# Optimization experiments

Hardware: AMD Instinct MI355X
Metric: run time of the kernel (lower is better)

## Reference

```python
import jax, jax.numpy as jnp
import numpy as np

NH, NKV, HD, H = 32, 8, 128, 4096
G = NH // NKV  # GQA group size = 4
EPS = 1e-5
SCALE = HD ** -0.5


def rms_norm(x, w, eps=EPS):
    # per-head RMSNorm over last dim, computed in fp32
    xf = x.astype(jnp.float32)
    var = jnp.mean(xf * xf, axis=-1, keepdims=True)
    return (w * (xf * jax.lax.rsqrt(var + eps)).astype(x.dtype))


def setup_inputs() -> dict:
    key = jax.random.key(0)
    ks = jax.random.split(key, 4)
    B, SQ, SKV = 4, 1024, 1601
    return {
        "hidden_states": jax.random.normal(ks[0], (B, SQ, H), jnp.float32),
        "cross_attention_states": jax.random.normal(ks[1], (B, SKV, H), jnp.float32),
        "wqkv": jax.random.normal(ks[2], ((NH + 2 * NKV) * HD, H), jnp.float32) * 0.02,
        "wo": jax.random.normal(ks[3], (NH * HD, H), jnp.float32) * 0.02,
        "q_norm_weight": jnp.ones((HD,), jnp.float32),
        "k_norm_weight": jnp.ones((HD,), jnp.float32),
    }


def reference(hidden_states, cross_attention_states, wqkv, wo, q_norm_weight, k_norm_weight):
    B, SQ, _ = hidden_states.shape
    SKV = cross_attention_states.shape[1]
    q_sz, kv_sz = NH * HD, NKV * HD

    # fused QKV projection on decoder tokens -> keep only q
    qkv_dec = jnp.einsum('bsh,oh->bso', hidden_states, wqkv)
    q = qkv_dec[..., :q_sz]
    # fused QKV projection on encoder tokens -> keep only k, v
    qkv_enc = jnp.einsum('bsh,oh->bso', cross_attention_states, wqkv)
    k = qkv_enc[..., q_sz:q_sz + kv_sz]
    v = qkv_enc[..., q_sz + kv_sz:]

    q = rms_norm(q.reshape(B, SQ, NH, HD), q_norm_weight)      # [B,SQ,NH,HD]
    k = rms_norm(k.reshape(B, SKV, NKV, HD), k_norm_weight)    # [B,SKV,NKV,HD]
    v = v.reshape(B, SKV, NKV, HD)

    # GQA: group query heads per kv head
    qg = q.reshape(B, SQ, NKV, G, HD)
    scores = jnp.einsum('bqkgd,bskd->bkgqs', qg, k) * SCALE    # [B,NKV,G,SQ,SKV]
    probs = jax.nn.softmax(scores, axis=-1)
    out = jnp.einsum('bkgqs,bskd->bqkgd', probs, v)            # [B,SQ,NKV,G,HD]
    out = out.reshape(B, SQ, NH * HD)
    return jnp.einsum('bso,ho->bsh', out, wo.T.T) if False else jnp.einsum('bsf,hf->bsh', out, wo)
```

## Files before the change

kernel.cpp:

```cpp
#include <hip/hip_runtime.h>
#include <cstdint>
#include <math.h>

typedef _Float16 f16;
typedef __attribute__((ext_vector_type(4))) _Float16 f16x4;
typedef __attribute__((ext_vector_type(8))) _Float16 f16x8;
typedef __attribute__((ext_vector_type(4))) float f32x4;

__device__ inline void gload_lds16(const void* g, void* l) {
  auto gp = reinterpret_cast<const __attribute__((address_space(1))) uint32_t*>(
      reinterpret_cast<uintptr_t>(g));
  auto lp = reinterpret_cast<__attribute__((address_space(3))) uint32_t*>(
      reinterpret_cast<uintptr_t>(l));
  __builtin_amdgcn_global_load_lds(gp, lp, 16 , 0, 0);
}

__device__ inline float wave_sum64(float v) {
#pragma unroll
  for (int m = 1; m < 64; m <<= 1) v += __shfl_xor(v, m);
  return v;
}

__global__ __launch_bounds__(256) void cvt_kernel(const float* __restrict__ src,
                                                  f16* __restrict__ dst, int n4) {
  int idx = blockIdx.x * blockDim.x + threadIdx.x;
  int stride = gridDim.x * blockDim.x;
  for (int i = idx; i < n4; i += stride) {
    float4 v = reinterpret_cast<const float4*>(src)[i];
    f16x4 h;
    h.x = (f16)v.x; h.y = (f16)v.y; h.z = (f16)v.z; h.w = (f16)v.w;
    reinterpret_cast<f16x4*>(dst)[i] = h;
  }
}

template <bool MB, int EPI>
__global__ __launch_bounds__(512, 2) void gemm256(const f16* __restrict__ A,
                                                  const f16* __restrict__ Bw,
                                                  float* __restrict__ C,
                                                  f16* __restrict__ Ch,
                                                  const float* __restrict__ wvec,
                                                  int M, int N, int K) {
  __shared__ f16 As[2][256][64];
  __shared__ f16 Bs[2][256][64];
  const int tid = threadIdx.x;
  const int l = tid & 63, w = tid >> 6;
  const int lq = l & 15, lk = l >> 4;
  const int wm = w >> 2, wn = w & 3;
  const int nwg = gridDim.x * gridDim.y;
  const int p = blockIdx.y * gridDim.x + blockIdx.x;
  const int L = (p & 7) * (nwg >> 3) + (p >> 3);
  const int bx = L % gridDim.x, by = L / gridDim.x;
  const int brow = by * 256, bcol = bx * 256;
  const int KT = K >> 6;

  const int srow8 = w * 8 + (l >> 3);
  const int scol  = ((l & 7) ^ (l >> 3)) * 8;
  const int swz   = (lq & 7) << 4;

  f32x4 acc[8][4];
  f32x4 zf = {0.f, 0.f, 0.f, 0.f};
#pragma unroll
  for (int m = 0; m < 8; ++m)
#pragma unroll
    for (int n = 0; n < 4; ++n) acc[m][n] = zf;

  auto stageA = [&](int kt, int buf, int i) {
    int ra = brow + i * 64 + srow8;
    if (MB) ra = (ra < M) ? ra : (M - 1);
    gload_lds16(A + (size_t)ra * K + kt * 64 + scol,
                (char*)(&As[buf][0][0]) + i * 8192 + w * 1024);
  };
  auto stageB = [&](int kt, int buf, int i) {
    int rb = bcol + i * 64 + srow8;
    gload_lds16(Bw + (size_t)rb * K + kt * 64 + scol,
                (char*)(&Bs[buf][0][0]) + i * 8192 + w * 1024);
  };
  auto ldA = [&](int buf, int m, int kk) -> f16x8 {
    int r = wm * 128 + m * 16 + lq;
    return *reinterpret_cast<const f16x8*>(
        (char*)(&As[buf][0][0]) + r * 128 + ((kk * 64 + lk * 16) ^ swz));
  };
  auto ldB = [&](int buf, int n, int kk) -> f16x8 {
    int r = wn * 64 + n * 16 + lq;
    return *reinterpret_cast<const f16x8*>(
        (char*)(&Bs[buf][0][0]) + r * 128 + ((kk * 64 + lk * 16) ^ swz));
  };

#pragma unroll
  for (int i = 0; i < 4; ++i) stageA(0, 0, i);
#pragma unroll
  for (int i = 0; i < 4; ++i) stageB(0, 0, i);

  f16x8 av[4][2], bv[2][2];
  for (int t = 0; t < KT; ++t) {
    const int buf = t & 1, nbuf = buf ^ 1;
    const bool pf = (t + 1 < KT);

    if (pf) { stageA(t + 1, nbuf, 0); stageA(t + 1, nbuf, 1); }
    if (pf) asm volatile("s_waitcnt vmcnt(2)" ::: "memory");
    else    asm volatile("s_waitcnt vmcnt(0)" ::: "memory");
    __builtin_amdgcn_s_barrier();
#pragma unroll
    for (int mm = 0; mm < 4; ++mm)
#pragma unroll
      for (int kk = 0; kk < 2; ++kk) av[mm][kk] = ldA(buf, mm, kk);
#pragma unroll
    for (int nn = 0; nn < 2; ++nn)
#pragma unroll
      for (int kk = 0; kk < 2; ++kk) bv[nn][kk] = ldB(buf, nn, kk);
    __builtin_amdgcn_s_setprio(1);
#pragma unroll
    for (int mm = 0; mm < 4; ++mm)
#pragma unroll
      for (int nn = 0; nn < 2; ++nn)
#pragma unroll
        for (int kk = 0; kk < 2; ++kk)
          acc[mm][nn] = __builtin_amdgcn_mfma_f32_16x16x32_f16(av[mm][kk], bv[nn][kk], acc[mm][nn], 0, 0, 0);
    __builtin_amdgcn_s_setprio(0);
    asm volatile("" ::: "memory");
    __builtin_amdgcn_s_barrier();

#pragma unroll
    for (int mm = 0; mm < 4; ++mm)
#pragma unroll
      for (int kk = 0; kk < 2; ++kk) av[mm][kk] = ldA(buf, 4 + mm, kk);
    if (pf) { stageA(t + 1, nbuf, 2); stageA(t + 1, nbuf, 3); }
    asm volatile("" ::: "memory");
    __builtin_amdgcn_s_barrier();
    __builtin_amdgcn_s_setprio(1);
#pragma unroll
    for (int mm = 0; mm < 4; ++mm)
#pragma unroll
      for (int nn = 0; nn < 2; ++nn)
#pragma unroll
        for (int kk = 0; kk < 2; ++kk)
          acc[4 + mm][nn] = __builtin_amdgcn_mfma_f32_16x16x32_f16(av[mm][kk], bv[nn][kk], acc[4 + mm][nn], 0, 0, 0);
    __builtin_amdgcn_s_setprio(0);
    asm volatile("" ::: "memory");
    __builtin_amdgcn_s_barrier();

#pragma unroll
    for (int nn = 0; nn < 2; ++nn)
#pragma unroll
      for (int kk = 0; kk < 2; ++kk) bv[nn][kk] = ldB(buf, 2 + nn, kk);
    if (pf) { stageB(t + 1, nbuf, 0); stageB(t + 1, nbuf, 1); }
    asm volatile("" ::: "memory");
    __builtin_amdgcn_s_barrier();
    __builtin_amdgcn_s_setprio(1);
#pragma unroll
    for (int mm = 0; mm < 4; ++mm)
#pragma unroll
      for (int nn = 0; nn < 2; ++nn)
#pragma unroll
        for (int kk = 0; kk < 2; ++kk)
          acc[4 + mm][2 + nn] = __builtin_amdgcn_mfma_f32_16x16x32_f16(av[mm][kk], bv[nn][kk], acc[4 + mm][2 + nn], 0, 0, 0);
    __builtin_amdgcn_s_setprio(0);
    asm volatile("" ::: "memory");
    __builtin_amdgcn_s_barrier();

#pragma unroll
    for (int mm = 0; mm < 4; ++mm)
#pragma unroll
      for (int kk = 0; kk < 2; ++kk) av[mm][kk] = ldA(buf, mm, kk);
    if (pf) { stageB(t + 1, nbuf, 2); stageB(t + 1, nbuf, 3); }
    asm volatile("" ::: "memory");
    __builtin_amdgcn_s_barrier();
    __builtin_amdgcn_s_setprio(1);
#pragma unroll
    for (int mm = 0; mm < 4; ++mm)
#pragma unroll
      for (int nn = 0; nn < 2; ++nn)
#pragma unroll
        for (int kk = 0; kk < 2; ++kk)
          acc[mm][2 + nn] = __builtin_amdgcn_mfma_f32_16x16x32_f16(av[mm][kk], bv[nn][kk], acc[mm][2 + nn], 0, 0, 0);
    __builtin_amdgcn_s_setprio(0);
    asm volatile("" ::: "memory");
    __builtin_amdgcn_s_barrier();
  }

  if (EPI == 0) {
#pragma unroll
    for (int m = 0; m < 8; ++m) {
#pragma unroll
      for (int j = 0; j < 4; ++j) {
        int row = brow + wm * 128 + m * 16 + lk * 4 + j;
        if (MB && row >= M) continue;
        float* dst = C + (size_t)row * N + bcol + wn * 64 + lq;
#pragma unroll
        for (int n = 0; n < 4; ++n) dst[n * 16] = acc[m][n][j];
      }
    }
  } else {
    __shared__ float ssq[256][4];
#pragma unroll
    for (int m = 0; m < 8; ++m)
#pragma unroll
      for (int j = 0; j < 4; ++j) {
        int lr = wm * 128 + m * 16 + lk * 4 + j;
        float pp = 0.f;
#pragma unroll
        for (int n = 0; n < 4; ++n) pp += acc[m][n][j] * acc[m][n][j];
        pp += __shfl_xor(pp, 1);
        pp += __shfl_xor(pp, 2);
        pp += __shfl_xor(pp, 4);
        pp += __shfl_xor(pp, 8);
        if (lq == 0) ssq[lr][wn] = pp;
      }
    asm volatile("" ::: "memory");
    __builtin_amdgcn_s_barrier();
    const int hh = wn >> 1;
    float wv[4];
#pragma unroll
    for (int n = 0; n < 4; ++n) wv[n] = wvec[(wn * 64 + n * 16 + lq) & 127];
#pragma unroll
    for (int m = 0; m < 8; ++m)
#pragma unroll
      for (int j = 0; j < 4; ++j) {
        int lr = wm * 128 + m * 16 + lk * 4 + j;
        float ss = ssq[lr][hh * 2] + ssq[lr][hh * 2 + 1];
        float rs = rsqrtf(ss * (1.0f / 128.0f) + 1e-5f) *
                   (0.08838834764831845f * 1.4426950408889634f);
        f16* dst = Ch + (size_t)(brow + lr) * N + bcol + wn * 64 + lq;
#pragma unroll
        for (int n = 0; n < 4; ++n) dst[n * 16] = (f16)(acc[m][n][j] * rs * wv[n]);
      }
  }
}

__global__ __launch_bounds__(256) void kvscatter_kernel(const float* __restrict__ KVraw,
                                                        const float* __restrict__ wk,
                                                        f16* __restrict__ Kf,
                                                        f16* __restrict__ Vtf) {
  const int w = threadIdx.x >> 6, l = threadIdx.x & 63;
  const int gw = blockIdx.x * 4 + w;
  const int r = gw >> 3, kvh = gw & 7;
  const int b = r / 1601, s = r - b * 1601;
  const float* kr = KVraw + (size_t)r * 2048 + kvh * 128;
  float2 kx = reinterpret_cast<const float2*>(kr)[l];
  float ss = wave_sum64(kx.x * kx.x + kx.y * kx.y);
  float rs = rsqrtf(ss * (1.0f / 128.0f) + 1e-5f);
  float2 wv = reinterpret_cast<const float2*>(wk)[l];
  union { f16 h[2]; unsigned u; } pk;
  pk.h[0] = (f16)(kx.x * rs * wv.x);
  pk.h[1] = (f16)(kx.y * rs * wv.y);
  reinterpret_cast<unsigned*>(Kf + ((size_t)(b * 8 + kvh) * 1664 + s) * 128)[l] = pk.u;
  const float* vr = kr + 1024;
  float2 vx = reinterpret_cast<const float2*>(vr)[l];
  f16* vcol = Vtf + ((size_t)(b * 8 + kvh) * 128 + l * 2) * 1664 + s;
  vcol[0] = (f16)vx.x;
  vcol[1664] = (f16)vx.y;
}

__global__ __launch_bounds__(512, 4) void attn_kernel(const f16* __restrict__ Qf,
                                                      const f16* __restrict__ Kf,
                                                      const f16* __restrict__ Vtf,
                                                      f16* __restrict__ Oa) {
  __shared__ f16 Ksm[2][64][128];
  __shared__ f16 Vsm[2][128][64];
  __shared__ f16 Psm[8][16][64];
  const int p = blockIdx.x;
  const int L = (p & 7) * 128 + (p >> 3);
  const int qt = L & 7, h = (L >> 3) & 31, b = L >> 8;
  const int kvh = h >> 2;
  const int tid = threadIdx.x;
  const int l = tid & 63, w = tid >> 6;
  const int lq = l & 15, lk = l >> 4;

  f16x8 qreg[4];
  const f16* Qbase = Qf + ((size_t)(b * 1024 + qt * 128 + w * 16)) * 4096 + h * 128;
#pragma unroll
  for (int ks = 0; ks < 4; ++ks)
    qreg[ks] = *reinterpret_cast<const f16x8*>(
        Qbase + (size_t)lq * 4096 + ks * 32 + lk * 8);

  const f16* Kb = Kf + (size_t)(b * 8 + kvh) * (1664 * 128);
  const f16* Vb = Vtf + (size_t)(b * 8 + kvh) * (128 * 1664);

  f32x4 o[8];
  f32x4 zf = {0.f, 0.f, 0.f, 0.f};
#pragma unroll
  for (int dn = 0; dn < 8; ++dn) o[dn] = zf;
  float mrow[4], lrow[4];
#pragma unroll
  for (int j = 0; j < 4; ++j) { mrow[j] = -1e30f; lrow[j] = 0.f; }

  char* Pw = (char*)(&Psm[w][0][0]);
  const int swzR = (lq & 7) << 4;

  auto stageK = [&](int t, int buf) {
#pragma unroll
    for (int i = 0; i < 2; ++i) {
      int row = w * 8 + i * 4 + lk;
      int cb = (lq * 16) ^ ((row & 7) << 4);
      gload_lds16(Kb + (size_t)(t * 64 + row) * 128 + (cb >> 1),
                  (char*)(&Ksm[buf][0][0]) + w * 2048 + i * 1024);
    }
  };
  auto stageV = [&](int t, int buf) {
#pragma unroll
    for (int i = 0; i < 2; ++i) {
      int r = w * 16 + i * 8 + (l >> 3);
      int cb = ((l & 7) * 16) ^ ((r & 7) << 4);
      gload_lds16(Vb + (size_t)r * 1664 + t * 64 + (cb >> 1),
                  (char*)(&Vsm[buf][0][0]) + w * 2048 + i * 1024);
    }
  };

  stageK(0, 0);
  stageV(0, 0);
  int cur = 0;
  for (int t = 0; t < 26; ++t) {
    if (t < 25) {
      stageK(t + 1, cur ^ 1);
      stageV(t + 1, cur ^ 1);
      asm volatile("s_waitcnt vmcnt(4)" ::: "memory");
    } else {
      asm volatile("s_waitcnt vmcnt(0)" ::: "memory");
    }
    __builtin_amdgcn_s_barrier();

    f32x4 s[4];
#pragma unroll
    for (int kn = 0; kn < 4; ++kn) s[kn] = zf;
    __builtin_amdgcn_s_setprio(1);
#pragma unroll
    for (int ks = 0; ks < 4; ++ks) {
      f16x8 bf[4];
#pragma unroll
      for (int kn = 0; kn < 4; ++kn)
        bf[kn] = *reinterpret_cast<const f16x8*>(
            (char*)(&Ksm[cur][0][0]) + (kn * 16 + lq) * 256 + ((ks * 64 + lk * 16) ^ swzR));
#pragma unroll
      for (int kn = 0; kn < 4; ++kn)
        s[kn] = __builtin_amdgcn_mfma_f32_16x16x32_f16(qreg[ks], bf[kn], s[kn], 0, 0, 0);
    }
    __builtin_amdgcn_s_setprio(0);

    if (t == 25) {
#pragma unroll
      for (int kn = 0; kn < 4; ++kn) {
        bool valid = (kn * 16 + lq) < 1;
#pragma unroll
        for (int j = 0; j < 4; ++j) s[kn][j] = valid ? s[kn][j] : -1e30f;
      }
    }

#pragma unroll
    for (int j = 0; j < 4; ++j) {
      float mt = fmaxf(fmaxf(s[0][j], s[1][j]), fmaxf(s[2][j], s[3][j]));
      mt = fmaxf(mt, __shfl_xor(mt, 1));
      mt = fmaxf(mt, __shfl_xor(mt, 2));
      mt = fmaxf(mt, __shfl_xor(mt, 4));
      mt = fmaxf(mt, __shfl_xor(mt, 8));
      float mo = mrow[j];
      if (mt > mo + 8.0f) {
        float corr = exp2f(mo - mt);
        mrow[j] = mt;
        lrow[j] *= corr;
#pragma unroll
        for (int dn = 0; dn < 8; ++dn) o[dn][j] *= corr;
        mo = mt;
      }
      float rsum = 0.f;
#pragma unroll
      for (int kn = 0; kn < 4; ++kn) {
        float pv = exp2f(s[kn][j] - mo);
        s[kn][j] = pv;
        rsum += pv;
      }
      lrow[j] += rsum;
      int prow = lk * 4 + j;
      int swzW = (prow & 7) << 4;
#pragma unroll
      for (int kn = 0; kn < 4; ++kn)
        *reinterpret_cast<f16*>(Pw + prow * 128 + (((kn * 16 + lq) * 2) ^ swzW)) =
            (f16)s[kn][j];
    }

    __builtin_amdgcn_s_setprio(1);
#pragma unroll
    for (int c = 0; c < 2; ++c) {
      f16x8 pa = *reinterpret_cast<const f16x8*>(
          Pw + lq * 128 + ((c * 64 + lk * 16) ^ swzR));
      f16x8 vb[8];
#pragma unroll
      for (int dn = 0; dn < 8; ++dn)
        vb[dn] = *reinterpret_cast<const f16x8*>(
            (char*)(&Vsm[cur][0][0]) + (dn * 16 + lq) * 128 + ((c * 64 + lk * 16) ^ swzR));
#pragma unroll
      for (int dn = 0; dn < 8; ++dn)
        o[dn] = __builtin_amdgcn_mfma_f32_16x16x32_f16(pa, vb[dn], o[dn], 0, 0, 0);
    }
    __builtin_amdgcn_s_setprio(0);
    __builtin_amdgcn_s_barrier();
    cur ^= 1;
  }

#pragma unroll
  for (int j = 0; j < 4; ++j) {
    float fl = lrow[j];
    fl += __shfl_xor(fl, 1);
    fl += __shfl_xor(fl, 2);
    fl += __shfl_xor(fl, 4);
    fl += __shfl_xor(fl, 8);
    float il = 1.0f / fl;
    int token = b * 1024 + qt * 128 + w * 16 + lk * 4 + j;
    f16* dst = Oa + (size_t)token * 4096 + h * 128;
#pragma unroll
    for (int dn = 0; dn < 8; ++dn) dst[dn * 16 + lq] = (f16)(o[dn][j] * il);
  }
}

extern "C" void kernel_launch(void* const* d_in, const int* in_sizes, int n_in,
                              void* d_out, int out_size, void* d_ws, size_t ws_size,
                              hipStream_t stream) {
  const float* hidden = (const float*)d_in[0];
  const float* cross  = (const float*)d_in[1];
  const float* wqkv   = (const float*)d_in[2];
  const float* wo     = (const float*)d_in[3];
  const float* qw     = (const float*)d_in[4];
  const float* kw     = (const float*)d_in[5];

  char* ws = (char*)d_ws;
  f16* hidden_h = (f16*)(ws + 0);
  f16* attn_h   = hidden_h;
  f16* wqkv_h = (f16*)(ws + 33554432);
  f16* cross_h = (f16*)(ws + 83886080);
  f16* k_h     = cross_h;
  f16* vt_h    = (f16*)(ws + 83886080 + 13631488);
  float* kvraw = (float*)(ws + 136347648);
  f16* wo_h    = (f16*)(ws + 136347648);
  f16* q_h = (f16*)d_out;

  cvt_kernel<<<2048, 256, 0, stream>>>(hidden, hidden_h, 16777216 / 4);
  cvt_kernel<<<2048, 256, 0, stream>>>(cross, cross_h, 26230784 / 4);
  cvt_kernel<<<2048, 256, 0, stream>>>(wqkv, wqkv_h, 25165824 / 4);
  gemm256<true, 0><<<dim3(8, 26), 512, 0, stream>>>(
      cross_h, wqkv_h + (size_t)4096 * 4096, kvraw, nullptr, nullptr, 6404, 2048, 4096);
  hipMemsetAsync(ws + 83886080, 0, 27262976, stream);
  kvscatter_kernel<<<12808, 256, 0, stream>>>(kvraw, kw, k_h, vt_h);
  cvt_kernel<<<2048, 256, 0, stream>>>(wo, wo_h, 16777216 / 4);
  gemm256<false, 1><<<dim3(16, 16), 512, 0, stream>>>(
      hidden_h, wqkv_h, nullptr, q_h, qw, 4096, 4096, 4096);
  attn_kernel<<<1024, 512, 0, stream>>>(q_h, k_h, vt_h, attn_h);
  gemm256<false, 0><<<dim3(16, 16), 512, 0, stream>>>(
      attn_h, wo_h, (float*)d_out, nullptr, nullptr, 4096, 4096, 4096);
}
```

Before: 685.1 us.

## Fuse K/V norm and scatter into GEMM epilogue and merge conversion launches

The KV projection GEMM epilogue now applies the K RMSNorm and writes K and transposed V directly in fp16 layout. This removes the fp32 intermediate buffer and the separate scatter kernel. The three fp32-to-fp16 conversions and the memset are merged into one kernel. The epilogue's V stores are strided, and register pressure in the GEMM may rise.

```diff
diff --git a/kernel.cpp b/kernel.cpp
--- a/kernel.cpp
+++ b/kernel.cpp
@@ -15,10 +15,23 @@
   __builtin_amdgcn_global_load_lds(gp, lp, 16 , 0, 0);
 }
 
-__device__ inline float wave_sum64(float v) {
-#pragma unroll
-  for (int m = 1; m < 64; m <<= 1) v += __shfl_xor(v, m);
-  return v;
+__global__ __launch_bounds__(256) void cvtzero_kernel(const float* __restrict__ s0, f16* __restrict__ d0,
+                                                      const float* __restrict__ s1, f16* __restrict__ d1,
+                                                      const float* __restrict__ s2, f16* __restrict__ d2,
+                                                      float4* __restrict__ z) {
+  int idx = blockIdx.x * blockDim.x + threadIdx.x;
+  int stride = gridDim.x * blockDim.x;
+  for (int i = idx; i < 18747392; i += stride) {
+    const float* src; f16* dst; int k;
+    if (i < 4194304) { src = s0; dst = d0; k = i; }
+    else if (i < 10752000) { src = s1; dst = d1; k = i - 4194304; }
+    else if (i < 17043456) { src = s2; dst = d2; k = i - 10752000; }
+    else { float4 zr = {0.f, 0.f, 0.f, 0.f}; z[i - 17043456] = zr; continue; }
+    float4 v = reinterpret_cast<const float4*>(src)[k];
+    f16x4 h;
+    h.x = (f16)v.x; h.y = (f16)v.y; h.z = (f16)v.z; h.w = (f16)v.w;
+    reinterpret_cast<f16x4*>(dst)[k] = h;
+  }
 }
 
 __global__ __launch_bounds__(256) void cvt_kernel(const float* __restrict__ src,
@@ -39,6 +52,7 @@
                                                   float* __restrict__ C,
                                                   f16* __restrict__ Ch,
                                                   const float* __restrict__ wvec,
+                                                  f16* __restrict__ Vtf,
                                                   int M, int N, int K) {
   __shared__ f16 As[2][256][64];
   __shared__ f16 Bs[2][256][64];
@@ -190,7 +204,7 @@
         for (int n = 0; n < 4; ++n) dst[n * 16] = acc[m][n][j];
       }
     }
-  } else {
+  } else if (EPI == 1) {
     __shared__ float ssq[256][4];
 #pragma unroll
     for (int m = 0; m < 8; ++m)
@@ -224,31 +238,65 @@
 #pragma unroll
         for (int n = 0; n < 4; ++n) dst[n * 16] = (f16)(acc[m][n][j] * rs * wv[n]);
       }
-  }
-}
-
-__global__ __launch_bounds__(256) void kvscatter_kernel(const float* __restrict__ KVraw,
-                                                        const float* __restrict__ wk,
-                                                        f16* __restrict__ Kf,
-                                                        f16* __restrict__ Vtf) {
-  const int w = threadIdx.x >> 6, l = threadIdx.x & 63;
-  const int gw = blockIdx.x * 4 + w;
-  const int r = gw >> 3, kvh = gw & 7;
-  const int b = r / 1601, s = r - b * 1601;
-  const float* kr = KVraw + (size_t)r * 2048 + kvh * 128;
-  float2 kx = reinterpret_cast<const float2*>(kr)[l];
-  float ss = wave_sum64(kx.x * kx.x + kx.y * kx.y);
-  float rs = rsqrtf(ss * (1.0f / 128.0f) + 1e-5f);
-  float2 wv = reinterpret_cast<const float2*>(wk)[l];
-  union { f16 h[2]; unsigned u; } pk;
-  pk.h[0] = (f16)(kx.x * rs * wv.x);
-  pk.h[1] = (f16)(kx.y * rs * wv.y);
-  reinterpret_cast<unsigned*>(Kf + ((size_t)(b * 8 + kvh) * 1664 + s) * 128)[l] = pk.u;
-  const float* vr = kr + 1024;
-  float2 vx = reinterpret_cast<const float2*>(vr)[l];
-  f16* vcol = Vtf + ((size_t)(b * 8 + kvh) * 128 + l * 2) * 1664 + s;
-  vcol[0] = (f16)vx.x;
-  vcol[1664] = (f16)vx.y;
+  } else {
+    const bool isK = (bcol < 1024);
+    __shared__ float ssq[256][4];
+    if (isK) {
+#pragma unroll
+      for (int m = 0; m < 8; ++m)
+#pragma unroll
+        for (int j = 0; j < 4; ++j) {
+          int lr = wm * 128 + m * 16 + lk * 4 + j;
+          float pp = 0.f;
+#pragma unroll
+          for (int n = 0; n < 4; ++n) pp += acc[m][n][j] * acc[m][n][j];
+          pp += __shfl_xor(pp, 1);
+          pp += __shfl_xor(pp, 2);
+          pp += __shfl_xor(pp, 4);
+          pp += __shfl_xor(pp, 8);
+          if (lq == 0) ssq[lr][wn] = pp;
+        }
+      asm volatile("" ::: "memory");
+      __builtin_amdgcn_s_barrier();
+    }
+    const int hh = wn >> 1;
+    float wv[4];
+    if (isK) {
+#pragma unroll
+      for (int n = 0; n < 4; ++n) wv[n] = wvec[(wn * 64 + n * 16 + lq) & 127];
+    }
+#pragma unroll
+    for (int m = 0; m < 8; ++m) {
+#pragma unroll
+      for (int j = 0; j < 4; ++j) {
+        int lr = wm * 128 + m * 16 + lk * 4 + j;
+        int r = brow + lr;
+        if (r >= M) continue;
+        unsigned bb = (unsigned)r / 1601u;
+        unsigned s = (unsigned)r - bb * 1601u;
+        if (isK) {
+          float ss = ssq[lr][hh * 2] + ssq[lr][hh * 2 + 1];
+          float rs = rsqrtf(ss * (1.0f / 128.0f) + 1e-5f);
+#pragma unroll
+          for (int n = 0; n < 4; ++n) {
+            int col = wn * 64 + n * 16 + lq;
+            int kvh = (bcol + col) >> 7;
+            int d = col & 127;
+            Ch[((size_t)(bb * 8 + kvh) * 1664 + s) * 128 + d] =
+                (f16)(acc[m][n][j] * rs * wv[n]);
+          }
+        } else {
+#pragma unroll
+          for (int n = 0; n < 4; ++n) {
+            int col = bcol - 1024 + wn * 64 + n * 16 + lq;
+            int kvh = col >> 7;
+            int d = col & 127;
+            Vtf[((size_t)(bb * 8 + kvh) * 128 + d) * 1664 + s] = (f16)acc[m][n][j];
+          }
+        }
+      }
+    }
+  }
 }
 
 __global__ __launch_bounds__(512, 4) void attn_kernel(const f16* __restrict__ Qf,
@@ -426,23 +474,19 @@
   f16* attn_h   = hidden_h;
   f16* wqkv_h = (f16*)(ws + 33554432);
   f16* cross_h = (f16*)(ws + 83886080);
-  f16* k_h     = cross_h;
-  f16* vt_h    = (f16*)(ws + 83886080 + 13631488);
-  float* kvraw = (float*)(ws + 136347648);
-  f16* wo_h    = (f16*)(ws + 136347648);
+  f16* wo_h    = (f16*)(ws + 83886080);
+  f16* k_h  = (f16*)(ws + 136347648);
+  f16* vt_h = (f16*)(ws + 136347648 + 13631488);
   f16* q_h = (f16*)d_out;
 
-  cvt_kernel<<<2048, 256, 0, stream>>>(hidden, hidden_h, 16777216 / 4);
-  cvt_kernel<<<2048, 256, 0, stream>>>(cross, cross_h, 26230784 / 4);
-  cvt_kernel<<<2048, 256, 0, stream>>>(wqkv, wqkv_h, 25165824 / 4);
-  gemm256<true, 0><<<dim3(8, 26), 512, 0, stream>>>(
-      cross_h, wqkv_h + (size_t)4096 * 4096, kvraw, nullptr, nullptr, 6404, 2048, 4096);
-  hipMemsetAsync(ws + 83886080, 0, 27262976, stream);
-  kvscatter_kernel<<<12808, 256, 0, stream>>>(kvraw, kw, k_h, vt_h);
+  cvtzero_kernel<<<2048, 256, 0, stream>>>(hidden, hidden_h, cross, cross_h,
+                                           wqkv, wqkv_h, (float4*)(ws + 136347648));
+  gemm256<true, 2><<<dim3(8, 26), 512, 0, stream>>>(
+      cross_h, wqkv_h + (size_t)4096 * 4096, nullptr, k_h, kw, vt_h, 6404, 2048, 4096);
   cvt_kernel<<<2048, 256, 0, stream>>>(wo, wo_h, 16777216 / 4);
   gemm256<false, 1><<<dim3(16, 16), 512, 0, stream>>>(
-      hidden_h, wqkv_h, nullptr, q_h, qw, 4096, 4096, 4096);
+      hidden_h, wqkv_h, nullptr, q_h, qw, nullptr, 4096, 4096, 4096);
   attn_kernel<<<1024, 512, 0, stream>>>(q_h, k_h, vt_h, attn_h);
   gemm256<false, 0><<<dim3(16, 16), 512, 0, stream>>>(
-      attn_h, wo_h, (float*)d_out, nullptr, nullptr, 4096, 4096, 4096);
-}
+      attn_h, wo_h, (float*)d_out, nullptr, nullptr, nullptr, 4096, 4096, 4096);
+}
```

Result: faster. 671.0 us (-2.1%).
